# Kernel optimization log

Hardware: AMD Instinct MI355X
Metric: run time of the kernel (lower is better)

## Reference

```python
import jax, jax.numpy as jnp
import numpy as np

OUT_DIM = 64
N_NODES = 50000
N_EDGES = 1000000


def setup_inputs() -> dict:
    key = jax.random.key(0)
    k1, k2, k3, k4, k5, k6 = jax.random.split(key, 6)
    return {
        "G_h": jax.random.normal(k1, (N_NODES, OUT_DIM), dtype=jnp.float32),
        "K_h": jax.random.normal(k2, (N_NODES, OUT_DIM), dtype=jnp.float32),
        "Q_h": jax.random.normal(k3, (N_NODES, OUT_DIM), dtype=jnp.float32),
        "V_h": jax.random.normal(k4, (N_NODES, 1, OUT_DIM), dtype=jnp.float32),
        "src": jax.random.randint(k5, (N_EDGES,), 0, N_NODES, dtype=jnp.int64),
        "dst": jax.random.randint(k6, (N_EDGES,), 0, N_NODES, dtype=jnp.int64),
    }


def reference(G_h, K_h, Q_h, V_h, src, dst):
    inv_sqrt_d = 1.0 / np.sqrt(OUT_DIM).astype(np.float32)
    # edge-wise gather of node features
    diff = G_h[src] - G_h[dst]                                   # [E, D]
    dist = -jnp.sqrt(jnp.sum(diff * diff, axis=-1) + 1e-6)       # [E]
    distance = jnp.exp(jnp.clip(dist * inv_sqrt_d, -5.0, 5.0))   # [E]
    score = jnp.sum(K_h[src] * Q_h[dst], axis=-1)                # [E]
    score_e = jnp.exp(jnp.clip(score * inv_sqrt_d, -5.0, 5.0))   # [E]
    weight = (score_e * distance)[:, None, None]                 # [E,1,1]
    v1_h = weight * V_h[src]                                     # [E,1,D]
    return v1_h
```

## Files before the change

### kernel.cpp

```cpp
#include <hip/hip_runtime.h>
#include <math.h>

#define N_NODES 50000
#define OUT_DIM 64

__global__ __launch_bounds__(256) void edge_message_kernel(
    const float* __restrict__ G,
    const float* __restrict__ K,
    const float* __restrict__ Q,
    const float* __restrict__ V,
    const int* __restrict__ src,
    const int* __restrict__ dst,
    float* __restrict__ out,
    int nEdges)
{
    const int lane = threadIdx.x & 63;
    const int wavesPerBlock = blockDim.x >> 6;
    const int waveId = blockIdx.x * wavesPerBlock + (threadIdx.x >> 6);
    const int waveStride = gridDim.x * wavesPerBlock;
    const float inv_sqrt_d = 0.125f;

    for (int e = waveId; e < nEdges; e += waveStride) {
        const int s = __builtin_nontemporal_load(&src[e]);
        const int d = __builtin_nontemporal_load(&dst[e]);

        const float gs = G[s * OUT_DIM + lane];
        const float gd = G[d * OUT_DIM + lane];
        const float ks = K[s * OUT_DIM + lane];
        const float qd = Q[d * OUT_DIM + lane];
        const float vs = V[s * OUT_DIM + lane];

        const float df = gs - gd;
        float a = df * df;
        float b = ks * qd;

        #pragma unroll
        for (int off = 32; off > 0; off >>= 1) {
            a += __shfl_xor(a, off, 64);
            b += __shfl_xor(b, off, 64);
        }

        const float dist  = -sqrtf(a + 1e-6f);
        float t1 = dist * inv_sqrt_d;
        t1 = fminf(fmaxf(t1, -5.0f), 5.0f);
        float t2 = b * inv_sqrt_d;
        t2 = fminf(fmaxf(t2, -5.0f), 5.0f);
        const float w = expf(t1) * expf(t2);

        __builtin_nontemporal_store(w * vs, &out[(size_t)e * OUT_DIM + lane]);
    }
}

extern "C" void kernel_launch(void* const* d_in, const int* in_sizes, int n_in,
                              void* d_out, int out_size, void* d_ws, size_t ws_size,
                              hipStream_t stream)
{
    const float* G   = (const float*)d_in[0];
    const float* K   = (const float*)d_in[1];
    const float* Q   = (const float*)d_in[2];
    const float* V   = (const float*)d_in[3];
    const int*   src = (const int*)d_in[4];
    const int*   dst = (const int*)d_in[5];
    float* out = (float*)d_out;

    const int nEdges = in_sizes[4];

    const int block = 256;
    const int wavesPerBlock = block / 64;
    int grid = (nEdges + wavesPerBlock - 1) / wavesPerBlock;
    if (grid > 2048) grid = 2048;

    edge_message_kernel<<<grid, block, 0, stream>>>(G, K, Q, V, src, dst, out, nEdges);
}
```

Baseline: 469.5 us.

## Process four edges per wavefront with float4 vectorized gathers and stores

Each 64-lane wave now handles four edges at once, with 16 lanes per edge each loading a float4 of the 64-wide rows. This gives 128-bit loads and stores instead of 32-bit ones, cuts each shuffle reduction from six steps to four, and loads four index pairs per wave iteration, raising memory-level parallelism in this gather-heavy kernel. The two exponentials are merged into one fast __expf of the summed arguments, which slightly changes precision. A tail guard clamps out-of-range indices and masks the store.

Measured after the change: 444.4 us. 1.06x faster.

```diff
diff --git a/kernel.cpp b/kernel.cpp
--- a/kernel.cpp
+++ b/kernel.cpp
@@ -3,6 +3,8 @@
 
 #define N_NODES 50000
 #define OUT_DIM 64
+
+typedef float f32x4 __attribute__((ext_vector_type(4)));
 
 __global__ __launch_bounds__(256) void edge_message_kernel(
     const float* __restrict__ G,
@@ -14,40 +16,56 @@
     float* __restrict__ out,
     int nEdges)
 {
-    const int lane = threadIdx.x & 63;
+    const int tid  = threadIdx.x;
+    const int lane = tid & 63;
+    const int grp  = lane >> 4;
+    const int sub  = lane & 15;
     const int wavesPerBlock = blockDim.x >> 6;
-    const int waveId = blockIdx.x * wavesPerBlock + (threadIdx.x >> 6);
+    const int waveId = blockIdx.x * wavesPerBlock + (tid >> 6);
     const int waveStride = gridDim.x * wavesPerBlock;
+
+    const f32x4* __restrict__ G4 = (const f32x4*)G;
+    const f32x4* __restrict__ K4 = (const f32x4*)K;
+    const f32x4* __restrict__ Q4 = (const f32x4*)Q;
+    const f32x4* __restrict__ V4 = (const f32x4*)V;
+    f32x4* __restrict__ out4 = (f32x4*)out;
+
     const float inv_sqrt_d = 0.125f;
 
-    for (int e = waveId; e < nEdges; e += waveStride) {
-        const int s = __builtin_nontemporal_load(&src[e]);
-        const int d = __builtin_nontemporal_load(&dst[e]);
+    for (int base = waveId * 4; base < nEdges; base += waveStride * 4) {
+        const int e = base + grp;
+        const bool valid = (e < nEdges);
+        const int ec = valid ? e : (nEdges - 1);
 
-        const float gs = G[s * OUT_DIM + lane];
-        const float gd = G[d * OUT_DIM + lane];
-        const float ks = K[s * OUT_DIM + lane];
-        const float qd = Q[d * OUT_DIM + lane];
-        const float vs = V[s * OUT_DIM + lane];
+        const int s = __builtin_nontemporal_load(&src[ec]);
+        const int d = __builtin_nontemporal_load(&dst[ec]);
 
-        const float df = gs - gd;
-        float a = df * df;
-        float b = ks * qd;
+        const f32x4 gs = G4[s * 16 + sub];
+        const f32x4 gd = G4[d * 16 + sub];
+        const f32x4 ks = K4[s * 16 + sub];
+        const f32x4 qd = Q4[d * 16 + sub];
+        const f32x4 vs = V4[s * 16 + sub];
+
+        const f32x4 df = gs - gd;
+        const f32x4 kq = ks * qd;
+        float a = df.x * df.x + df.y * df.y + df.z * df.z + df.w * df.w;
+        float b = kq.x + kq.y + kq.z + kq.w;
 
         #pragma unroll
-        for (int off = 32; off > 0; off >>= 1) {
+        for (int off = 8; off > 0; off >>= 1) {
             a += __shfl_xor(a, off, 64);
             b += __shfl_xor(b, off, 64);
         }
 
-        const float dist  = -sqrtf(a + 1e-6f);
-        float t1 = dist * inv_sqrt_d;
+        float t1 = -sqrtf(a + 1e-6f) * inv_sqrt_d;
         t1 = fminf(fmaxf(t1, -5.0f), 5.0f);
         float t2 = b * inv_sqrt_d;
         t2 = fminf(fmaxf(t2, -5.0f), 5.0f);
-        const float w = expf(t1) * expf(t2);
+        const float w = __expf(t1 + t2);
 
-        __builtin_nontemporal_store(w * vs, &out[(size_t)e * OUT_DIM + lane]);
+        if (valid) {
+            __builtin_nontemporal_store(w * vs, &out4[(size_t)e * 16 + sub]);
+        }
     }
 }
 
@@ -66,8 +84,8 @@
     const int nEdges = in_sizes[4];
 
     const int block = 256;
-    const int wavesPerBlock = block / 64;
-    int grid = (nEdges + wavesPerBlock - 1) / wavesPerBlock;
+    const int edgesPerBlock = (block / 64) * 4;
+    int grid = (nEdges + edgesPerBlock - 1) / edgesPerBlock;
     if (grid > 2048) grid = 2048;
 
     edge_message_kernel<<<grid, block, 0, stream>>>(G, K, Q, V, src, dst, out, nEdges);
```
